# Performance work log

Hardware: AMD Instinct MI355X
Metric: run time of the kernel (lower is better)

The kernel has to match this reference:

```python
import jax, jax.numpy as jnp
import numpy as np

EPS = 1e-5
C_M, C, C_Z = 256, 32, 128
N_SEQ, N_RES = 256, 1024


def setup_inputs() -> dict:
    key = jax.random.key(0)
    k1, k2, k3 = jax.random.split(key, 3)
    msa = jax.random.normal(k1, (N_SEQ, N_RES, C_M), dtype=jnp.float32)
    norm_w = jnp.ones((C_M,), dtype=jnp.float32)
    norm_b = jnp.zeros((C_M,), dtype=jnp.float32)
    w_ab = jax.random.normal(k2, (C, C_M), dtype=jnp.float32) * (1.0 / np.sqrt(C_M))
    b_ab = jnp.zeros((C,), dtype=jnp.float32)
    w_out = jax.random.normal(k3, (C_Z, C * C), dtype=jnp.float32) * (1.0 / C)
    b_out = jnp.zeros((C_Z,), dtype=jnp.float32)
    return {"msa": msa, "norm_w": norm_w, "norm_b": norm_b,
            "w_ab": w_ab, "b_ab": b_ab, "w_out": w_out, "b_out": b_out}


def reference(msa, norm_w, norm_b, w_ab, b_ab, w_out, b_out):
    # msa: (s, r, c_m) -> (r, s, c_m)
    x = jnp.transpose(msa, (1, 0, 2))
    s = x.shape[1]
    # LayerNorm over c_m
    mu = jnp.mean(x, axis=-1, keepdims=True)
    var = jnp.mean(jnp.square(x - mu), axis=-1, keepdims=True)
    xn = (x - mu) * jax.lax.rsqrt(var + EPS) * norm_w + norm_b
    # a == b: same linear applied twice to same input in the original
    a = jnp.einsum('rsm,cm->rsc', xn, w_ab) + b_ab          # (r, s, c)
    # mean over s of outer product == batched A^T A / s  -> (r, c, c)
    o = jnp.einsum('rsx,rsy->rxy', a, a) / s
    o = o.reshape(o.shape[0], C * C)                        # (r, c*c)
    pre_pair = jnp.einsum('rk,zk->rz', o, w_out) + b_out    # (r, c_z)
    r = pre_pair.shape[0]
    # unsqueeze(1).expand(r, r, c_z)
    pair = jnp.broadcast_to(pre_pair[:, None, :], (r, r, C_Z))
    return pair
```

## Files before the change

### kernel.cpp

```cpp
#include <hip/hip_runtime.h>

#define NSEQ 256
#define NRES 1024
#define CM   256
#define CC   32
#define CZ   128
#define EPS  1e-5f
#define SROW (NRES * CM)
#define MCH  16
#define XPAD 20

typedef float f4v __attribute__((ext_vector_type(4)));

__global__ void opm_setup(const float* __restrict__ nw,
                          const float* __restrict__ nb,
                          const float* __restrict__ w_ab,
                          const float* __restrict__ b_ab,
                          float* __restrict__ wt_g,
                          float* __restrict__ k12)
{
    __shared__ float wls[CM * CC];
    const int t = threadIdx.x;
    const float nwm = nw[t];
    #pragma unroll
    for (int c = 0; c < CC; ++c)
        wls[t * CC + c] = nwm * w_ab[c * CM + t];
    __syncthreads();
    for (int i = t; i < CM * CC; i += 256) wt_g[i] = wls[i];
    if (t < CC) {
        float k1 = 0.f, k2 = 0.f;
        for (int m = 0; m < CM; ++m) {
            k1 += wls[m * CC + t];
            k2 = fmaf(nb[m], w_ab[t * CM + m], k2);
        }
        k12[t]      = k1;
        k12[CC + t] = k2 + b_ab[t];
    }
}

__launch_bounds__(256, 2)
__global__ void opm_compute(const float* __restrict__ msa,
                            const float* __restrict__ wt_g,
                            const float* __restrict__ k12,
                            const float* __restrict__ w_out,
                            const float* __restrict__ b_out,
                            float* __restrict__ pre_out)
{
    __shared__ float wt[CM * CC];
    __shared__ float xa[2][NSEQ * XPAD];

    const int tid  = threadIdx.x;
    const int r    = blockIdx.x;
    const int wave = tid >> 6;

    const int sc4 = tid & 3;
    const int sg4 = tid >> 2;
    const int sc8 = tid & 7;
    const int sg8 = tid >> 3;
    const int c0  = sc8 << 2;

    const float* xr = msa + (size_t)r * CM + (sc4 << 2);

    #pragma unroll
    for (int k = 0; k < 8; ++k) {
        const int i = (tid + (k << 8)) << 2;
        *(float4*)&wt[i] = *(const float4*)&wt_g[i];
    }

    float G[8][4];
    #pragma unroll
    for (int j = 0; j < 8; ++j) {
        G[j][0] = 0.f; G[j][1] = 0.f; G[j][2] = 0.f; G[j][3] = 0.f;
    }
    float psum[4], pssq[4];

    float4 pf[4];
    #pragma unroll
    for (int k = 0; k < 4; ++k)
        pf[k] = *(const float4*)(xr + (size_t)(sg4 + (k << 6)) * SROW);
    #pragma unroll
    for (int k = 0; k < 4; ++k) {
        *(float4*)&xa[0][(sg4 + (k << 6)) * XPAD + (sc4 << 2)] = pf[k];
        psum[k] = (pf[k].x + pf[k].y) + (pf[k].z + pf[k].w);
        pssq[k] = fmaf(pf[k].x, pf[k].x, fmaf(pf[k].y, pf[k].y,
                  fmaf(pf[k].z, pf[k].z, pf[k].w * pf[k].w)));
    }
    #pragma unroll
    for (int k = 0; k < 4; ++k)
        pf[k] = *(const float4*)(xr + (size_t)(sg4 + (k << 6)) * SROW + MCH);
    __syncthreads();

    float* bR = xa[0];
    float* bW = xa[1];
    for (int mb = 0; mb < CM; mb += MCH) {
        const int nxt = mb + MCH;
        if (nxt < CM) {
            #pragma unroll
            for (int k = 0; k < 4; ++k) {
                *(float4*)&bW[(sg4 + (k << 6)) * XPAD + (sc4 << 2)] = pf[k];
                psum[k] += (pf[k].x + pf[k].y) + (pf[k].z + pf[k].w);
                pssq[k]  = fmaf(pf[k].x, pf[k].x, fmaf(pf[k].y, pf[k].y,
                           fmaf(pf[k].z, pf[k].z, fmaf(pf[k].w, pf[k].w, pssq[k]))));
            }
            if (nxt + MCH < CM) {
                #pragma unroll
                for (int k = 0; k < 4; ++k)
                    pf[k] = *(const float4*)(xr + (size_t)(sg4 + (k << 6)) * SROW + (nxt + MCH));
            }
        }
        #pragma unroll
        for (int mm = 0; mm < MCH; mm += 4) {
            const float4 w0 = *(const float4*)&wt[(mb + mm + 0) * CC + c0];
            const float4 w1 = *(const float4*)&wt[(mb + mm + 1) * CC + c0];
            const float4 w2 = *(const float4*)&wt[(mb + mm + 2) * CC + c0];
            const float4 w3 = *(const float4*)&wt[(mb + mm + 3) * CC + c0];
            #pragma unroll
            for (int j = 0; j < 8; ++j) {
                const float4 x4 = *(const float4*)&bR[(sg8 + (j << 5)) * XPAD + mm];
                G[j][0] = fmaf(x4.x, w0.x, fmaf(x4.y, w1.x, fmaf(x4.z, w2.x, fmaf(x4.w, w3.x, G[j][0]))));
                G[j][1] = fmaf(x4.x, w0.y, fmaf(x4.y, w1.y, fmaf(x4.z, w2.y, fmaf(x4.w, w3.y, G[j][1]))));
                G[j][2] = fmaf(x4.x, w0.z, fmaf(x4.y, w1.z, fmaf(x4.z, w2.z, fmaf(x4.w, w3.z, G[j][2]))));
                G[j][3] = fmaf(x4.x, w0.w, fmaf(x4.y, w1.w, fmaf(x4.z, w2.w, fmaf(x4.w, w3.w, G[j][3]))));
            }
        }
        __syncthreads();
        float* t = bR; bR = bW; bW = t;
    }

    #pragma unroll
    for (int k = 0; k < 4; ++k) {
        float s1 = psum[k], s2 = pssq[k];
        s1 += __shfl_xor(s1, 1); s1 += __shfl_xor(s1, 2);
        s2 += __shfl_xor(s2, 1); s2 += __shfl_xor(s2, 2);
        if (sc4 == 0) {
            const int s = sg4 + (k << 6);
            const float mu  = s1 * (1.f / CM);
            const float var = s2 * (1.f / CM) - mu * mu;
            xa[0][s]        = mu;
            xa[0][NSEQ + s] = 1.f / sqrtf(var + EPS);
        }
    }
    __syncthreads();

    {
        const float4 k1v = *(const float4*)&k12[c0];
        const float4 k2v = *(const float4*)&k12[CC + c0];
        #pragma unroll
        for (int j = 0; j < 8; ++j) {
            const int s = sg8 + (j << 5);
            const float mu = xa[0][s], rstd = xa[0][NSEQ + s];
            float4 av;
            av.x = fmaf(rstd, G[j][0] - mu * k1v.x, k2v.x);
            av.y = fmaf(rstd, G[j][1] - mu * k1v.y, k2v.y);
            av.z = fmaf(rstd, G[j][2] - mu * k1v.z, k2v.z);
            av.w = fmaf(rstd, G[j][3] - mu * k1v.w, k2v.w);
            *(float4*)&wt[s * CC + ((sc8 ^ (s & 7)) << 2)] = av;
        }
    }
    __syncthreads();

    const int grp = wave;
    const int xs  = (tid >> 3) & 7;
    const int ys  = tid & 7;
    float4 pr0 = {0,0,0,0}, pr1 = {0,0,0,0}, pr2 = {0,0,0,0}, pr3 = {0,0,0,0};
    #pragma unroll 4
    for (int si = 0; si < 64; ++si) {
        const int s  = (grp << 6) + si;
        const int sw = si & 7;
        const float4 ax = *(const float4*)&wt[s * CC + ((xs ^ sw) << 2)];
        const float4 ay = *(const float4*)&wt[s * CC + ((ys ^ sw) << 2)];
        pr0.x = fmaf(ax.x, ay.x, pr0.x); pr0.y = fmaf(ax.x, ay.y, pr0.y);
        pr0.z = fmaf(ax.x, ay.z, pr0.z); pr0.w = fmaf(ax.x, ay.w, pr0.w);
        pr1.x = fmaf(ax.y, ay.x, pr1.x); pr1.y = fmaf(ax.y, ay.y, pr1.y);
        pr1.z = fmaf(ax.y, ay.z, pr1.z); pr1.w = fmaf(ax.y, ay.w, pr1.w);
        pr2.x = fmaf(ax.z, ay.x, pr2.x); pr2.y = fmaf(ax.z, ay.y, pr2.y);
        pr2.z = fmaf(ax.z, ay.z, pr2.z); pr2.w = fmaf(ax.z, ay.w, pr2.w);
        pr3.x = fmaf(ax.w, ay.x, pr3.x); pr3.y = fmaf(ax.w, ay.y, pr3.y);
        pr3.z = fmaf(ax.w, ay.z, pr3.z); pr3.w = fmaf(ax.w, ay.w, pr3.w);
    }
    {
        float* pb = &xa[0][(grp << 10) + (xs << 7) + (ys << 2)];
        *(float4*)&pb[0 << 5] = pr0;
        *(float4*)&pb[1 << 5] = pr1;
        *(float4*)&pb[2 << 5] = pr2;
        *(float4*)&pb[3 << 5] = pr3;
    }
    __syncthreads();
    {
        const float inv_s = 1.f / NSEQ;
        float4 acc = *(const float4*)&xa[0][(tid << 2)];
        const float4 b1 = *(const float4*)&xa[0][1024 + (tid << 2)];
        const float4 b2 = *(const float4*)&xa[0][2048 + (tid << 2)];
        const float4 b3 = *(const float4*)&xa[0][3072 + (tid << 2)];
        acc.x = (acc.x + b1.x + b2.x + b3.x) * inv_s;
        acc.y = (acc.y + b1.y + b2.y + b3.y) * inv_s;
        acc.z = (acc.z + b1.z + b2.z + b3.z) * inv_s;
        acc.w = (acc.w + b1.w + b2.w + b3.w) * inv_s;
        *(float4*)&xa[0][tid << 2] = acc;
    }
    __syncthreads();

    {
        const int z    = tid & 127;
        const int half = tid >> 7;
        const float* wrow = w_out + (size_t)z * (CC * CC) + half * 512;
        const float* op   = &xa[0][half * 512];
        float po = 0.f;
        #pragma unroll 8
        for (int k = 0; k < 512; k += 4) {
            const float4 o4 = *(const float4*)&op[k];
            const float4 w4 = *(const float4*)&wrow[k];
            po = fmaf(o4.x, w4.x, fmaf(o4.y, w4.y, fmaf(o4.z, w4.z, fmaf(o4.w, w4.w, po))));
        }
        xa[0][4096 + (half << 7) + z] = po;
    }
    __syncthreads();
    if (tid < CZ)
        pre_out[(size_t)r * CZ + tid] = xa[0][4096 + tid] + xa[0][4096 + CZ + tid] + b_out[tid];
}

__launch_bounds__(256, 8)
__global__ void opm_bcast(const float* __restrict__ pre,
                          float* __restrict__ out)
{
    const int bid = blockIdx.x;
    const int r   = bid >> 3;
    const int jb  = bid & 7;
    const int z4  = threadIdx.x & 31;
    const int jo  = threadIdx.x >> 5;

    const f4v pv = *((const f4v*)(pre + (size_t)r * CZ) + z4);
    f4v* outp = (f4v*)out + ((size_t)r * NRES + (size_t)jb * 128) * (CZ / 4);
    for (int j0 = 0; j0 < 128; j0 += 8)
        __builtin_nontemporal_store(pv, &outp[(size_t)(j0 + jo) * (CZ / 4) + z4]);
}

extern "C" void kernel_launch(void* const* d_in, const int* in_sizes, int n_in,
                              void* d_out, int out_size, void* d_ws, size_t ws_size,
                              hipStream_t stream) {
    const float* msa   = (const float*)d_in[0];
    const float* nw    = (const float*)d_in[1];
    const float* nb    = (const float*)d_in[2];
    const float* w_ab  = (const float*)d_in[3];
    const float* b_ab  = (const float*)d_in[4];
    const float* w_out = (const float*)d_in[5];
    const float* b_out = (const float*)d_in[6];
    float* out = (float*)d_out;

    float* pre  = (float*)d_ws;
    float* wt_g = pre + (size_t)NRES * CZ;
    float* k12  = wt_g + CM * CC;

    opm_setup<<<1, 256, 0, stream>>>(nw, nb, w_ab, b_ab, wt_g, k12);
    opm_compute<<<NRES, 256, 0, stream>>>(msa, wt_g, k12, w_out, b_out, pre);
    opm_bcast<<<NRES * 8, 256, 0, stream>>>(pre, out);
}
```

Baseline: 802.9 us.

## Give each wave private LDS strips to drop per-chunk block barriers

The LDS staging buffer is split into per-wave strips: each wave loads and consumes only its own 64 sequence rows, so the block-wide __syncthreads inside the 16-chunk channel loop is removed. The row padding shrinks from 20 to 18, which reduces LDS footprint and changes the bank mapping. LayerNorm statistics move to a small separate array, and the swizzle indices are adjusted to the new row mapping. Without a barrier, correctness relies on intra-wave lockstep ordering of LDS writes and reads, and the float4 accesses on an 18-float stride may be less well aligned.

```diff
diff --git a/kernel.cpp b/kernel.cpp
--- a/kernel.cpp
+++ b/kernel.cpp
@@ -8,7 +8,8 @@
 #define EPS  1e-5f
 #define SROW (NRES * CM)
 #define MCH  16
-#define XPAD 20
+#define RS   18
+#define WSTRIP (64 * RS)
 
 typedef float f4v __attribute__((ext_vector_type(4)));
 
@@ -47,19 +48,25 @@
                             float* __restrict__ pre_out)
 {
     __shared__ float wt[CM * CC];
-    __shared__ float xa[2][NSEQ * XPAD];
-
-    const int tid  = threadIdx.x;
-    const int r    = blockIdx.x;
-    const int wave = tid >> 6;
-
-    const int sc4 = tid & 3;
-    const int sg4 = tid >> 2;
-    const int sc8 = tid & 7;
-    const int sg8 = tid >> 3;
-    const int c0  = sc8 << 2;
-
-    const float* xr = msa + (size_t)r * CM + (sc4 << 2);
+    __shared__ float xa[8 * WSTRIP];
+    __shared__ float st[512];
+
+    const int tid = threadIdx.x;
+    const int r   = blockIdx.x;
+    const int w   = tid >> 6;
+    const int l   = tid & 63;
+
+    const int sl = l & 3;
+    const int si = l >> 2;
+    const int q  = l >> 3;
+    const int c  = l & 7;
+    const int c0 = c << 2;
+
+    const int brow = (w << 3) + (si & 7) + ((si >> 3) << 5);
+    const float* xr = msa + (size_t)r * CM + (sl << 2);
+
+    float* s0 = &xa[w * WSTRIP];
+    float* s1 = &xa[(4 + w) * WSTRIP];
 
     #pragma unroll
     for (int k = 0; k < 8; ++k) {
@@ -69,35 +76,34 @@
 
     float G[8][4];
     #pragma unroll
-    for (int j = 0; j < 8; ++j) {
-        G[j][0] = 0.f; G[j][1] = 0.f; G[j][2] = 0.f; G[j][3] = 0.f;
-    }
+    for (int j = 0; j < 8; ++j) { G[j][0] = 0.f; G[j][1] = 0.f; G[j][2] = 0.f; G[j][3] = 0.f; }
     float psum[4], pssq[4];
 
     float4 pf[4];
     #pragma unroll
     for (int k = 0; k < 4; ++k)
-        pf[k] = *(const float4*)(xr + (size_t)(sg4 + (k << 6)) * SROW);
+        pf[k] = *(const float4*)(xr + (size_t)(brow + (k << 6)) * SROW);
     #pragma unroll
     for (int k = 0; k < 4; ++k) {
-        *(float4*)&xa[0][(sg4 + (k << 6)) * XPAD + (sc4 << 2)] = pf[k];
+        *(float4*)&s0[(si + (k << 4)) * RS + (sl << 2)] = pf[k];
         psum[k] = (pf[k].x + pf[k].y) + (pf[k].z + pf[k].w);
         pssq[k] = fmaf(pf[k].x, pf[k].x, fmaf(pf[k].y, pf[k].y,
                   fmaf(pf[k].z, pf[k].z, pf[k].w * pf[k].w)));
     }
     #pragma unroll
     for (int k = 0; k < 4; ++k)
-        pf[k] = *(const float4*)(xr + (size_t)(sg4 + (k << 6)) * SROW + MCH);
-    __syncthreads();
-
-    float* bR = xa[0];
-    float* bW = xa[1];
+        pf[k] = *(const float4*)(xr + (size_t)(brow + (k << 6)) * SROW + MCH);
+
+    __syncthreads();
+
+    float* bR = s0;
+    float* bW = s1;
     for (int mb = 0; mb < CM; mb += MCH) {
         const int nxt = mb + MCH;
         if (nxt < CM) {
             #pragma unroll
             for (int k = 0; k < 4; ++k) {
-                *(float4*)&bW[(sg4 + (k << 6)) * XPAD + (sc4 << 2)] = pf[k];
+                *(float4*)&bW[(si + (k << 4)) * RS + (sl << 2)] = pf[k];
                 psum[k] += (pf[k].x + pf[k].y) + (pf[k].z + pf[k].w);
                 pssq[k]  = fmaf(pf[k].x, pf[k].x, fmaf(pf[k].y, pf[k].y,
                            fmaf(pf[k].z, pf[k].z, fmaf(pf[k].w, pf[k].w, pssq[k]))));
@@ -105,7 +111,7 @@
             if (nxt + MCH < CM) {
                 #pragma unroll
                 for (int k = 0; k < 4; ++k)
-                    pf[k] = *(const float4*)(xr + (size_t)(sg4 + (k << 6)) * SROW + (nxt + MCH));
+                    pf[k] = *(const float4*)(xr + (size_t)(brow + (k << 6)) * SROW + (nxt + MCH));
             }
         }
         #pragma unroll
@@ -116,28 +122,27 @@
             const float4 w3 = *(const float4*)&wt[(mb + mm + 3) * CC + c0];
             #pragma unroll
             for (int j = 0; j < 8; ++j) {
-                const float4 x4 = *(const float4*)&bR[(sg8 + (j << 5)) * XPAD + mm];
+                const float4 x4 = *(const float4*)&bR[(q + (j << 3)) * RS + mm];
                 G[j][0] = fmaf(x4.x, w0.x, fmaf(x4.y, w1.x, fmaf(x4.z, w2.x, fmaf(x4.w, w3.x, G[j][0]))));
                 G[j][1] = fmaf(x4.x, w0.y, fmaf(x4.y, w1.y, fmaf(x4.z, w2.y, fmaf(x4.w, w3.y, G[j][1]))));
                 G[j][2] = fmaf(x4.x, w0.z, fmaf(x4.y, w1.z, fmaf(x4.z, w2.z, fmaf(x4.w, w3.z, G[j][2]))));
                 G[j][3] = fmaf(x4.x, w0.w, fmaf(x4.y, w1.w, fmaf(x4.z, w2.w, fmaf(x4.w, w3.w, G[j][3]))));
             }
         }
-        __syncthreads();
         float* t = bR; bR = bW; bW = t;
     }
 
     #pragma unroll
     for (int k = 0; k < 4; ++k) {
-        float s1 = psum[k], s2 = pssq[k];
-        s1 += __shfl_xor(s1, 1); s1 += __shfl_xor(s1, 2);
-        s2 += __shfl_xor(s2, 1); s2 += __shfl_xor(s2, 2);
-        if (sc4 == 0) {
-            const int s = sg4 + (k << 6);
-            const float mu  = s1 * (1.f / CM);
-            const float var = s2 * (1.f / CM) - mu * mu;
-            xa[0][s]        = mu;
-            xa[0][NSEQ + s] = 1.f / sqrtf(var + EPS);
+        float a1 = psum[k], a2 = pssq[k];
+        a1 += __shfl_xor(a1, 1); a1 += __shfl_xor(a1, 2);
+        a2 += __shfl_xor(a2, 1); a2 += __shfl_xor(a2, 2);
+        if (sl == 0) {
+            const int i = si + (k << 4);
+            const float mu  = a1 * (1.f / CM);
+            const float var = a2 * (1.f / CM) - mu * mu;
+            st[(w << 7) + i]      = mu;
+            st[(w << 7) + 64 + i] = 1.f / sqrtf(var + EPS);
         }
     }
     __syncthreads();
@@ -147,28 +152,30 @@
         const float4 k2v = *(const float4*)&k12[CC + c0];
         #pragma unroll
         for (int j = 0; j < 8; ++j) {
-            const int s = sg8 + (j << 5);
-            const float mu = xa[0][s], rstd = xa[0][NSEQ + s];
+            const int i = q + (j << 3);
+            const int s = (w << 3) + q + (j << 5);
+            const float mu   = st[(w << 7) + i];
+            const float rstd = st[(w << 7) + 64 + i];
             float4 av;
             av.x = fmaf(rstd, G[j][0] - mu * k1v.x, k2v.x);
             av.y = fmaf(rstd, G[j][1] - mu * k1v.y, k2v.y);
             av.z = fmaf(rstd, G[j][2] - mu * k1v.z, k2v.z);
             av.w = fmaf(rstd, G[j][3] - mu * k1v.w, k2v.w);
-            *(float4*)&wt[s * CC + ((sc8 ^ (s & 7)) << 2)] = av;
-        }
-    }
-    __syncthreads();
-
-    const int grp = wave;
-    const int xs  = (tid >> 3) & 7;
-    const int ys  = tid & 7;
+            *(float4*)&wt[s * CC + ((c ^ q) << 2)] = av;
+        }
+    }
+    __syncthreads();
+
+    const int grp = w;
+    const int xs_ = (tid >> 3) & 7;
+    const int ys_ = tid & 7;
     float4 pr0 = {0,0,0,0}, pr1 = {0,0,0,0}, pr2 = {0,0,0,0}, pr3 = {0,0,0,0};
     #pragma unroll 4
-    for (int si = 0; si < 64; ++si) {
-        const int s  = (grp << 6) + si;
-        const int sw = si & 7;
-        const float4 ax = *(const float4*)&wt[s * CC + ((xs ^ sw) << 2)];
-        const float4 ay = *(const float4*)&wt[s * CC + ((ys ^ sw) << 2)];
+    for (int si_ = 0; si_ < 64; ++si_) {
+        const int s  = (grp << 6) + si_;
+        const int sw = s & 7;
+        const float4 ax = *(const float4*)&wt[s * CC + ((xs_ ^ sw) << 2)];
+        const float4 ay = *(const float4*)&wt[s * CC + ((ys_ ^ sw) << 2)];
         pr0.x = fmaf(ax.x, ay.x, pr0.x); pr0.y = fmaf(ax.x, ay.y, pr0.y);
         pr0.z = fmaf(ax.x, ay.z, pr0.z); pr0.w = fmaf(ax.x, ay.w, pr0.w);
         pr1.x = fmaf(ax.y, ay.x, pr1.x); pr1.y = fmaf(ax.y, ay.y, pr1.y);
@@ -179,24 +186,24 @@
         pr3.z = fmaf(ax.w, ay.z, pr3.z); pr3.w = fmaf(ax.w, ay.w, pr3.w);
     }
     {
-        float* pb = &xa[0][(grp << 10) + (xs << 7) + (ys << 2)];
-        *(float4*)&pb[0 << 5] = pr0;
-        *(float4*)&pb[1 << 5] = pr1;
-        *(float4*)&pb[2 << 5] = pr2;
-        *(float4*)&pb[3 << 5] = pr3;
+        float* pb = &xa[(grp << 10) + ((xs_ << 2) * CC) + (ys_ << 2)];
+        *(float4*)&pb[0 * CC] = pr0;
+        *(float4*)&pb[1 * CC] = pr1;
+        *(float4*)&pb[2 * CC] = pr2;
+        *(float4*)&pb[3 * CC] = pr3;
     }
     __syncthreads();
     {
         const float inv_s = 1.f / NSEQ;
-        float4 acc = *(const float4*)&xa[0][(tid << 2)];
-        const float4 b1 = *(const float4*)&xa[0][1024 + (tid << 2)];
-        const float4 b2 = *(const float4*)&xa[0][2048 + (tid << 2)];
-        const float4 b3 = *(const float4*)&xa[0][3072 + (tid << 2)];
+        float4 acc = *(const float4*)&xa[(tid << 2)];
+        const float4 b1 = *(const float4*)&xa[1024 + (tid << 2)];
+        const float4 b2 = *(const float4*)&xa[2048 + (tid << 2)];
+        const float4 b3 = *(const float4*)&xa[3072 + (tid << 2)];
         acc.x = (acc.x + b1.x + b2.x + b3.x) * inv_s;
         acc.y = (acc.y + b1.y + b2.y + b3.y) * inv_s;
         acc.z = (acc.z + b1.z + b2.z + b3.z) * inv_s;
         acc.w = (acc.w + b1.w + b2.w + b3.w) * inv_s;
-        *(float4*)&xa[0][tid << 2] = acc;
+        *(float4*)&xa[tid << 2] = acc;
     }
     __syncthreads();
 
@@ -204,7 +211,7 @@
         const int z    = tid & 127;
         const int half = tid >> 7;
         const float* wrow = w_out + (size_t)z * (CC * CC) + half * 512;
-        const float* op   = &xa[0][half * 512];
+        const float* op   = &xa[half * 512];
         float po = 0.f;
         #pragma unroll 8
         for (int k = 0; k < 512; k += 4) {
@@ -212,11 +219,11 @@
             const float4 w4 = *(const float4*)&wrow[k];
             po = fmaf(o4.x, w4.x, fmaf(o4.y, w4.y, fmaf(o4.z, w4.z, fmaf(o4.w, w4.w, po))));
         }
-        xa[0][4096 + (half << 7) + z] = po;
+        xa[4096 + (half << 7) + z] = po;
     }
     __syncthreads();
     if (tid < CZ)
-        pre_out[(size_t)r * CZ + tid] = xa[0][4096 + tid] + xa[0][4096 + CZ + tid] + b_out[tid];
+        pre_out[(size_t)r * CZ + tid] = xa[4096 + tid] + xa[4096 + CZ + tid] + b_out[tid];
 }
 
 __launch_bounds__(256, 8)
```

Result: slower. 936.2 us (+16.6%).
